# Kernel optimization log

Measured on AMD Instinct MI355X. Metric: run time of the kernel, lower is better.

Reference implementation:

```python
import jax, jax.numpy as jnp
import numpy as np
from jax import lax

HEADS, DIM_HEAD = 4, 64
INNER = HEADS * DIM_HEAD              # 256
FEAT_DIM = MAP_DIM = OUT_DIM = 128
EXPANDED = 4 * OUT_DIM                # 512 (MBConv expansion)
MAP_SIZE = (8, 8, 8)
EPS = 1e-5


def conv3d(x, w, groups=1):
    # x: NCDHW, w: OIDHW ([out, in/groups, kd, kh, kw]); stride 1, 'same' padding
    return lax.conv_general_dilated(x, w, (1, 1, 1), 'SAME',
                                    feature_group_count=groups,
                                    dimension_numbers=('NCDHW', 'OIDHW', 'NCDHW'))


def inorm(x):
    # InstanceNorm3d (affine=False): normalize over spatial dims per sample/channel
    m = x.mean((2, 3, 4), keepdims=True)
    v = ((x - m) ** 2).mean((2, 3, 4), keepdims=True)
    return (x - m) * lax.rsqrt(v + EPS)


def _split_heads(t, spatial):
    # 'b (dim_head heads) d h w -> b heads (d h w) dim_head'
    B = t.shape[0]
    N = spatial[0] * spatial[1] * spatial[2]
    return t.reshape(B, DIM_HEAD, HEADS, N).transpose(0, 2, 3, 1)


def _merge_heads(t, spatial):
    # 'b heads n dim_head -> b (dim_head heads) d h w'
    B = t.shape[0]
    return t.transpose(0, 3, 1, 2).reshape(B, DIM_HEAD * HEADS, *spatial)


def setup_inputs() -> dict:
    key = jax.random.key(0)
    ks = jax.random.split(key, 16)
    r = lambda k, s: jax.random.normal(k, s, jnp.float32) * 0.05
    return {
        'x': jax.random.normal(ks[0], (2, FEAT_DIM, 24, 24, 24), jnp.float32),
        'semantic_map': jax.random.normal(ks[1], (2, MAP_DIM) + MAP_SIZE, jnp.float32),
        'w_fqv_dw': r(ks[2], (FEAT_DIM, 1, 3, 3, 3)),
        'w_fqv_pw': r(ks[3], (2 * INNER, FEAT_DIM, 1, 1, 1)),
        'w_mqv':    r(ks[4], (2 * INNER, MAP_DIM, 1, 1, 1)),
        'w_fout_dw': r(ks[5], (INNER, 1, 3, 3, 3)),
        'w_fout_pw': r(ks[6], (OUT_DIM, INNER, 1, 1, 1)),
        'w_mout':   r(ks[7], (MAP_DIM, INNER, 1, 1, 1)),
        'w_exp':    r(ks[8], (EXPANDED, OUT_DIM, 1, 1, 1)),
        'w_dw':     r(ks[9], (EXPANDED, 1, 3, 3, 3)),
        'w_se1':    r(ks[10], (EXPANDED // 4, EXPANDED, 1, 1, 1)),
        'b_se1':    jnp.zeros((EXPANDED // 4,), jnp.float32),
        'w_se2':    r(ks[11], (EXPANDED, EXPANDED // 4, 1, 1, 1)),
        'b_se2':    jnp.zeros((EXPANDED,), jnp.float32),
        'w_pw':     r(ks[12], (OUT_DIM, EXPANDED, 1, 1, 1)),
    }


def _mbconv(x, w_exp, w_dw, w_se1, b_se1, w_se2, b_se2, w_pw):
    # MBConv (preact ConvNormAct blocks, InstanceNorm + ReLU, SE, identity shortcut)
    h = conv3d(jax.nn.relu(inorm(x)), w_exp)
    h = conv3d(jax.nn.relu(inorm(h)), w_dw, groups=EXPANDED)
    s = h.mean((2, 3, 4), keepdims=True)                       # squeeze
    s = jax.nn.relu(conv3d(s, w_se1) + b_se1[None, :, None, None, None])
    s = jax.nn.sigmoid(conv3d(s, w_se2) + b_se2[None, :, None, None, None])
    h = h * s
    h = conv3d(inorm(h), w_pw)                                 # pointwise, act=False
    return h + x


def reference(x, semantic_map, w_fqv_dw, w_fqv_pw, w_mqv, w_fout_dw, w_fout_pw,
              w_mout, w_exp, w_dw, w_se1, b_se1, w_se2, b_se2, w_pw):
    B, C, D, H, W = x.shape
    feat = inorm(x)
    m = inorm(semantic_map)

    # QV projections: depthwise-separable for feat, 1x1 for map
    fqv = conv3d(conv3d(feat, w_fqv_dw, groups=FEAT_DIM), w_fqv_pw)
    fq, fv = jnp.split(fqv, 2, axis=1)
    mqv = conv3d(m, w_mqv)
    mq, mv = jnp.split(mqv, 2, axis=1)

    fq = _split_heads(fq, (D, H, W))   # [B, h, Nf, dh]
    fv = _split_heads(fv, (D, H, W))
    mq = _split_heads(mq, MAP_SIZE)    # [B, h, Nm, dh]
    mv = _split_heads(mv, MAP_SIZE)

    # shared score matrix, dual-direction softmax
    attn = jnp.einsum('bhid,bhjd->bhij', fq, mq) * (DIM_HEAD ** -0.5)
    feat_map_attn = jax.nn.softmax(attn, axis=-1)   # over map tokens j
    map_feat_attn = jax.nn.softmax(attn, axis=-2)   # over feat tokens i

    feat_out = jnp.einsum('bhij,bhjd->bhid', feat_map_attn, mv)   # [B,h,Nf,dh]
    map_out = jnp.einsum('bhji,bhjd->bhid', map_feat_attn, fv)    # [B,h,Nm,dh]

    feat_out = _merge_heads(feat_out, (D, H, W))
    map_out = _merge_heads(map_out, MAP_SIZE)

    feat_out = conv3d(conv3d(feat_out, w_fout_dw, groups=INNER), w_fout_pw)
    map_out = conv3d(map_out, w_mout)

    out = feat_out + x   # shortcut is identity (feat_dim == out_dim)
    out = _mbconv(out, w_exp, w_dw, w_se1, b_se1, w_se2, b_se2, w_pw)
    map_out = map_out + semantic_map
    return out, map_out
```

## Files before the change

kernel.cpp:

```cpp
#include <hip/hip_runtime.h>
#include <hip/hip_bf16.h>
#include <cstddef>

#define NF 13824
#define NM 512
#define NIC 27

typedef __attribute__((ext_vector_type(8))) short bf16x8;
typedef __attribute__((ext_vector_type(4))) float f32x4;

__device__ __forceinline__ float fexp2(float x){ return __builtin_amdgcn_exp2f(x); }

__device__ __forceinline__ void gload16(const float* g, float* l){
  __builtin_amdgcn_global_load_lds((const __attribute__((address_space(1))) void*)g,
                                   (__attribute__((address_space(3))) void*)l, 16, 0, 0);
}

__global__ void k_transpose6(const float* __restrict__ s0, float* __restrict__ d0,
                             const float* __restrict__ s1, float* __restrict__ d1,
                             const float* __restrict__ s2, float* __restrict__ d2,
                             const float* __restrict__ s3, float* __restrict__ d3,
                             const float* __restrict__ s4, float* __restrict__ d4,
                             const float* __restrict__ s5, float* __restrict__ d5){
  const float* W; float* WT; int Cout, Cin;
  switch (blockIdx.y){
    case 0: W=s0; WT=d0; Cout=512; Cin=128; break;
    case 1: W=s1; WT=d1; Cout=512; Cin=128; break;
    case 2: W=s2; WT=d2; Cout=128; Cin=256; break;
    case 3: W=s3; WT=d3; Cout=128; Cin=256; break;
    case 4: W=s4; WT=d4; Cout=512; Cin=128; break;
    default: W=s5; WT=d5; Cout=128; Cin=512; break;
  }
  int idx = blockIdx.x*256 + threadIdx.x;
  if (idx >= Cout*Cin) return;
  int co = idx / Cin, ci = idx % Cin;
  WT[(size_t)ci*Cout + co] = W[idx];
}

__global__ void k_stats(const float* __restrict__ in, float2* __restrict__ st, int N,
                        float2* __restrict__ tf){
  int row = blockIdx.x;
  const float* p = in + (size_t)row*N;
  float s=0.f, q=0.f;
  int n4 = N/4;
  for (int i=threadIdx.x; i<n4; i+=256){
    float4 v = *(const float4*)(p + i*4);
    s += v.x+v.y+v.z+v.w;
    q += v.x*v.x+v.y*v.y+v.z*v.z+v.w*v.w;
  }
  __shared__ float rs[256], rq[256];
  rs[threadIdx.x]=s; rq[threadIdx.x]=q;
  __syncthreads();
  for (int o=128;o>0;o>>=1){
    if (threadIdx.x<o){ rs[threadIdx.x]+=rs[threadIdx.x+o]; rq[threadIdx.x]+=rq[threadIdx.x+o]; }
    __syncthreads();
  }
  if (threadIdx.x==0){
    float m = rs[0]/N;
    float v = rq[0]/N - m*m;
    if (v<0.f) v=0.f;
    st[row] = make_float2(m, v);
    if (tf){
      float a = rsqrtf(v + 1e-5f);
      tf[row] = make_float2(a, -m*a);
    }
  }
}

__global__ void k_make_tf(const float2* __restrict__ st, const float* __restrict__ sbuf,
                          float2* __restrict__ tf, int rows){
  int i = blockIdx.x*256 + threadIdx.x;
  if (i>=rows) return;
  float s = sbuf ? sbuf[i] : 1.f;
  float2 mv = st[i];
  float a = s*rsqrtf(s*s*mv.y + 1e-5f);
  tf[i] = make_float2(a, -mv.x*a);
}

__global__ void k_red(const float2* __restrict__ part, int nparts, int rows,
                      float invN, float2* __restrict__ tf){
  int w = threadIdx.x>>6, l = threadIdx.x&63;
  int row = blockIdx.x*4 + w;
  if (row >= rows) return;
  const float2* p = part + (size_t)row*nparts;
  float s=0.f, q=0.f;
  for (int k=l; k<nparts; k+=64){ float2 v = p[k]; s += v.x; q += v.y; }
  s += __shfl_xor(s,1); s += __shfl_xor(s,2); s += __shfl_xor(s,4);
  s += __shfl_xor(s,8); s += __shfl_xor(s,16); s += __shfl_xor(s,32);
  q += __shfl_xor(q,1); q += __shfl_xor(q,2); q += __shfl_xor(q,4);
  q += __shfl_xor(q,8); q += __shfl_xor(q,16); q += __shfl_xor(q,32);
  if (l==0){
    float m = s*invN;
    float v = q*invN - m*m;
    if (v<0.f) v=0.f;
    float a = rsqrtf(v + 1e-5f);
    tf[row] = make_float2(a, -m*a);
  }
}

__global__ void k_act(const float* __restrict__ in, const float2* __restrict__ tf,
                      float* __restrict__ outp){
  int i = blockIdx.x*256 + threadIdx.x;
  int n4 = i*4;
  int bc = n4 / NF;
  float2 t = tf[bc];
  float4 v = *(const float4*)(in + n4);
  v.x = fmaxf(t.x*v.x + t.y, 0.f);
  v.y = fmaxf(t.x*v.y + t.y, 0.f);
  v.z = fmaxf(t.x*v.z + t.y, 0.f);
  v.w = fmaxf(t.x*v.w + t.y, 0.f);
  *(float4*)(outp + n4) = v;
}

__global__ void k_fold(const float* __restrict__ wt, const float2* __restrict__ tf,
                       float* __restrict__ wf, float* __restrict__ bias){
  int co = blockIdx.x;
  int b  = blockIdx.y;
  float partb = 0.f;
  for (int ci=threadIdx.x; ci<512; ci+=256){
    float w = wt[ci*128 + co];
    float2 t = tf[b*512 + ci];
    wf[((size_t)b*512 + ci)*128 + co] = w * t.x;
    partb += w * t.y;
  }
  __shared__ float red[256];
  red[threadIdx.x] = partb; __syncthreads();
  for (int o=128;o>0;o>>=1){ if (threadIdx.x<o) red[threadIdx.x]+=red[threadIdx.x+o]; __syncthreads(); }
  if (threadIdx.x==0) bias[b*128 + co] = red[0];
}

__global__ __launch_bounds__(256) void k_dw3t(const float* __restrict__ in, const float* __restrict__ w,
                      const float2* __restrict__ tf, float* __restrict__ out,
                      int C, int relu, float2* __restrict__ stout){
  int bc = blockIdx.x;
  int c = bc % C;
  __shared__ float lds[4 + 26*728];
  __shared__ float rs2[256], rq2[256];
  float a = 1.f, bb = 0.f;
  if (tf){ float2 t = tf[bc]; a=t.x; bb=t.y; }

  {
    float4* l4 = (float4*)lds;
    float4 z = make_float4(0.f,0.f,0.f,0.f);
    for (int i=threadIdx.x; i<(4+26*728)/4; i+=256) l4[i] = z;
  }
  __syncthreads();

  const float* pin = in + (size_t)bc*NF;
  for (int i=threadIdx.x; i<NF/4; i+=256){
    int n = i*4;
    int d = n/576, r2 = n%576;
    int h = r2/24, wq = r2%24;
    float4 v = *(const float4*)(pin + n);
    float v0 = a*v.x+bb, v1 = a*v.y+bb, v2 = a*v.z+bb, v3 = a*v.w+bb;
    if (relu){ v0=fmaxf(v0,0.f); v1=fmaxf(v1,0.f); v2=fmaxf(v2,0.f); v3=fmaxf(v3,0.f); }
    *(float4*)(lds + 4 + (d+1)*728 + (h+1)*28 + wq) = make_float4(v0,v1,v2,v3);
  }

  const float* wc = w + c*27;
  float wr[27];
  #pragma unroll
  for (int k=0;k<27;k++) wr[k] = wc[k];
  __syncthreads();

  float ss=0.f, sq=0.f;
  for (int r = threadIdx.x; r < 576; r += 256){
    int d = r/24, h = r%24;
    float acc[24];
    #pragma unroll
    for (int i=0;i<24;i++) acc[i] = 0.f;
    #pragma unroll
    for (int kd=0;kd<3;kd++){
      #pragma unroll
      for (int kh=0;kh<3;kh++){
        const float* row = lds + 4 + (d+kd)*728 + (h+kh)*28;
        float rr[24];
        #pragma unroll
        for (int q=0;q<6;q++){
          float4 v4 = *(const float4*)(row + 4*q);
          rr[4*q]=v4.x; rr[4*q+1]=v4.y; rr[4*q+2]=v4.z; rr[4*q+3]=v4.w;
        }
        float rl = row[-1];
        float rrgt = row[24];
        float w0 = wr[kd*9+kh*3+0], w1 = wr[kd*9+kh*3+1], w2 = wr[kd*9+kh*3+2];
        acc[0] += w0*rl + w1*rr[0] + w2*rr[1];
        #pragma unroll
        for (int i=1;i<23;i++) acc[i] += w0*rr[i-1] + w1*rr[i] + w2*rr[i+1];
        acc[23] += w0*rr[22] + w1*rr[23] + w2*rrgt;
      }
    }
    if (stout){
      #pragma unroll
      for (int i=0;i<24;i++){ ss += acc[i]; sq += acc[i]*acc[i]; }
    }
    float* op = out + (size_t)bc*NF + r*24;
    #pragma unroll
    for (int q=0;q<6;q++)
      *(float4*)(op + 4*q) = make_float4(acc[4*q],acc[4*q+1],acc[4*q+2],acc[4*q+3]);
  }
  if (stout){
    rs2[threadIdx.x]=ss; rq2[threadIdx.x]=sq;
    __syncthreads();
    for (int o=128;o>0;o>>=1){
      if (threadIdx.x<o){ rs2[threadIdx.x]+=rs2[threadIdx.x+o]; rq2[threadIdx.x]+=rq2[threadIdx.x+o]; }
      __syncthreads();
    }
    if (threadIdx.x==0){
      float m = rs2[0]/NF;
      float v = rq2[0]/NF - m*m;
      stout[bc] = make_float2(m, v>0.f? v:0.f);
    }
  }
}

__global__ __launch_bounds__(256) void k_pw2(const float* __restrict__ in, const float* __restrict__ Wt,
                    const float* __restrict__ bias,
                    int Cin, int Cout, int N, int wstride,
                    const float* __restrict__ res,
                    float* __restrict__ out0,
                    __hip_bfloat16* __restrict__ qnm, __hip_bfloat16* __restrict__ vdm,
                    int mode, float2* __restrict__ part, int nparts){
  int b = blockIdx.z;
  int n0 = blockIdx.x*64, co0 = blockIdx.y*128;
  int t = threadIdx.x;
  int tx = t & 15, tyy = t >> 4;
  int wv = t >> 6, ln = t & 63;
  __shared__ float wl[2][32*128];
  __shared__ float il[2][32*64];
  float acc[8][4] = {};
  const float* inb = in + (size_t)b*Cin*N;
  const float* wb  = Wt + (size_t)b*wstride;

  int wrow = (ln>>5), wcol = (ln&31)*4;
  int irow = (ln>>4), icol = (ln&15)*4;

  auto STAGE = [&](int c0, int buf){
    #pragma unroll
    for (int k=0;k<4;k++){
      int row = wv*8 + 2*k + wrow;
      gload16(wb + (size_t)(c0+row)*Cout + co0 + wcol, &wl[buf][row*128 + wcol]);
    }
    #pragma unroll
    for (int k=0;k<2;k++){
      int row = wv*8 + 4*k + irow;
      gload16(inb + (size_t)(c0+row)*N + n0 + icol, &il[buf][row*64 + icol]);
    }
  };

  STAGE(0, 0);
  __syncthreads();

  int nc = Cin >> 5;
  int cur = 0;
  for (int c=0; c<nc; c++){
    if (c+1 < nc) STAGE((c+1)*32, cur^1);
    #pragma unroll
    for (int ci=0;ci<32;ci++){
      const float* wr2 = &wl[cur][ci*128 + tyy*8];
      float4 w0 = *(const float4*)(wr2);
      float4 w1 = *(const float4*)(wr2+4);
      float4 b4 = *(const float4*)&il[cur][ci*64 + tx*4];
      acc[0][0]+=w0.x*b4.x; acc[0][1]+=w0.x*b4.y; acc[0][2]+=w0.x*b4.z; acc[0][3]+=w0.x*b4.w;
      acc[1][0]+=w0.y*b4.x; acc[1][1]+=w0.y*b4.y; acc[1][2]+=w0.y*b4.z; acc[1][3]+=w0.y*b4.w;
      acc[2][0]+=w0.z*b4.x; acc[2][1]+=w0.z*b4.y; acc[2][2]+=w0.z*b4.z; acc[2][3]+=w0.z*b4.w;
      acc[3][0]+=w0.w*b4.x; acc[3][1]+=w0.w*b4.y; acc[3][2]+=w0.w*b4.z; acc[3][3]+=w0.w*b4.w;
      acc[4][0]+=w1.x*b4.x; acc[4][1]+=w1.x*b4.y; acc[4][2]+=w1.x*b4.z; acc[4][3]+=w1.x*b4.w;
      acc[5][0]+=w1.y*b4.x; acc[5][1]+=w1.y*b4.y; acc[5][2]+=w1.y*b4.z; acc[5][3]+=w1.y*b4.w;
      acc[6][0]+=w1.z*b4.x; acc[6][1]+=w1.z*b4.y; acc[6][2]+=w1.z*b4.z; acc[6][3]+=w1.z*b4.w;
      acc[7][0]+=w1.w*b4.x; acc[7][1]+=w1.w*b4.y; acc[7][2]+=w1.w*b4.z; acc[7][3]+=w1.w*b4.w;
    }
    __syncthreads();
    cur ^= 1;
  }

  if (mode==0){
    #pragma unroll
    for (int i=0;i<8;i++){
      int co = co0 + tyy*8 + i;
      float bco = bias ? bias[b*Cout + co] : 0.f;
      float* op = out0 + ((size_t)b*Cout + co)*N;
      float sv=0.f, qv=0.f;
      #pragma unroll
      for (int j=0;j<4;j++){
        int n = n0 + tx*4 + j;
        float v = acc[i][j] + bco;
        if (res) v += res[((size_t)b*Cout + co)*N + n];
        op[n] = v;
        sv += v; qv += v*v;
      }
      if (part){
        sv += __shfl_xor(sv,1); sv += __shfl_xor(sv,2); sv += __shfl_xor(sv,4); sv += __shfl_xor(sv,8);
        qv += __shfl_xor(qv,1); qv += __shfl_xor(qv,2); qv += __shfl_xor(qv,4); qv += __shfl_xor(qv,8);
        if (tx==0)
          part[(size_t)(b*Cout + co)*nparts + blockIdx.x] = make_float2(sv, qv);
      }
    }
  } else {
    bool isq = (co0 < 256);
    #pragma unroll
    for (int i=0;i<8;i++){
      int co = co0 + tyy*8 + i;
      int head = co & 3, dd = (co & 255) >> 2;
      int bhid = b*4 + head;
      #pragma unroll
      for (int j=0;j<4;j++){
        int n = n0 + tx*4 + j;
        __hip_bfloat16 v = __float2bfloat16(acc[i][j]);
        if (isq) qnm[((size_t)bhid*N + n)*64 + dd] = v;
        else     vdm[((size_t)(bhid*64 + dd))*N + n] = v;
      }
    }
  }
}

__global__ __launch_bounds__(256) void k_pw2s(const float* __restrict__ in, const float* __restrict__ Wt,
                    const float* __restrict__ bias,
                    int Cin, int Cout, int N, int wstride,
                    const float* __restrict__ res,
                    float* __restrict__ out0,
                    int mode, float2* __restrict__ part, int nparts){
  int b = blockIdx.z;
  int n0 = blockIdx.x*64, co0 = blockIdx.y*64;
  int t = threadIdx.x;
  int tx = t & 15, ty = t >> 4;
  int wv = t >> 6, ln = t & 63;
  __shared__ float wl[2][32*64];
  __shared__ float il[2][32*64];
  float acc[4][4] = {};
  const float* inb = in + (size_t)b*Cin*N;
  const float* wb  = Wt + (size_t)b*wstride;

  int row4 = (ln>>4), col4 = (ln&15)*4;

  auto STAGE = [&](int c0, int buf){
    #pragma unroll
    for (int k=0;k<2;k++){
      int row = wv*8 + 4*k + row4;
      gload16(wb  + (size_t)(c0+row)*Cout + co0 + col4, &wl[buf][row*64 + col4]);
      gload16(inb + (size_t)(c0+row)*N    + n0  + col4, &il[buf][row*64 + col4]);
    }
  };

  STAGE(0, 0);
  __syncthreads();

  int nc = Cin >> 5;
  int cur = 0;
  for (int c=0; c<nc; c++){
    if (c+1 < nc) STAGE((c+1)*32, cur^1);
    #pragma unroll
    for (int ci=0;ci<32;ci++){
      float4 a4 = *(const float4*)&wl[cur][ci*64 + ty*4];
      float4 b4 = *(const float4*)&il[cur][ci*64 + tx*4];
      acc[0][0]+=a4.x*b4.x; acc[0][1]+=a4.x*b4.y; acc[0][2]+=a4.x*b4.z; acc[0][3]+=a4.x*b4.w;
      acc[1][0]+=a4.y*b4.x; acc[1][1]+=a4.y*b4.y; acc[1][2]+=a4.y*b4.z; acc[1][3]+=a4.y*b4.w;
      acc[2][0]+=a4.z*b4.x; acc[2][1]+=a4.z*b4.y; acc[2][2]+=a4.z*b4.z; acc[2][3]+=a4.z*b4.w;
      acc[3][0]+=a4.w*b4.x; acc[3][1]+=a4.w*b4.y; acc[3][2]+=a4.w*b4.z; acc[3][3]+=a4.w*b4.w;
    }
    __syncthreads();
    cur ^= 1;
  }

  #pragma unroll
  for (int i=0;i<4;i++){
    int co = co0 + ty*4 + i;
    float bco = bias ? bias[b*Cout + co] : 0.f;
    float* op = out0 + ((size_t)b*Cout + co)*N;
    float sv=0.f, qv=0.f;
    #pragma unroll
    for (int j=0;j<4;j++){
      int n = n0 + tx*4 + j;
      float v = acc[i][j] + bco;
      if (res) v += res[((size_t)b*Cout + co)*N + n];
      op[n] = v;
      sv += v; qv += v*v;
    }
    if (part){
      sv += __shfl_xor(sv,1); sv += __shfl_xor(sv,2); sv += __shfl_xor(sv,4); sv += __shfl_xor(sv,8);
      qv += __shfl_xor(qv,1); qv += __shfl_xor(qv,2); qv += __shfl_xor(qv,4); qv += __shfl_xor(qv,8);
      if (tx==0)
        part[(size_t)(b*Cout + co)*nparts + blockIdx.x] = make_float2(sv, qv);
    }
  }
  (void)mode;
}

__global__ __launch_bounds__(256) void k_pw(const float* __restrict__ in, const float* __restrict__ WT,
                    const float2* __restrict__ tf, int relu,
                    int Cin, int Cout, int N,
                    const float* __restrict__ res,
                    float* __restrict__ out0,
                    __hip_bfloat16* __restrict__ qnm, __hip_bfloat16* __restrict__ vdm,
                    int mode){
  int b = blockIdx.z;
  int n0 = blockIdx.x*64, co0 = blockIdx.y*64;
  int tx = threadIdx.x & 15, ty = threadIdx.x >> 4;
  int cc = threadIdx.x & 63, g = threadIdx.x >> 6;
  __shared__ float wl[32][68];
  __shared__ float il[32][68];
  float acc[4][4] = {};
  const float* inb = in + (size_t)b*Cin*N;

  float rw[8], rv[8], ta[8], tb[8];
  #pragma unroll
  for (int rr=0;rr<8;rr++){ ta[rr]=1.f; tb[rr]=0.f; }
  #pragma unroll
  for (int rr=0;rr<8;rr++){
    int ci = g + 4*rr;
    rw[rr] = WT[(size_t)ci*Cout + co0 + cc];
    rv[rr] = inb[(size_t)ci*N + n0 + cc];
    if (tf){ float2 t = tf[b*Cin + ci]; ta[rr]=t.x; tb[rr]=t.y; }
  }

  for (int c0=0;c0<Cin;c0+=32){
    __syncthreads();
    #pragma unroll
    for (int rr=0;rr<8;rr++){
      int ci = g + 4*rr;
      wl[ci][cc] = rw[rr];
      float v = ta[rr]*rv[rr] + tb[rr];
      if (relu) v = fmaxf(v, 0.f);
      il[ci][cc] = v;
    }
    __syncthreads();
    if (c0+32 < Cin){
      int c0n = c0+32;
      #pragma unroll
      for (int rr=0;rr<8;rr++){
        int ci = g + 4*rr;
        rw[rr] = WT[(size_t)(c0n+ci)*Cout + co0 + cc];
        rv[rr] = inb[(size_t)(c0n+ci)*N + n0 + cc];
        if (tf){ float2 t = tf[b*Cin + c0n + ci]; ta[rr]=t.x; tb[rr]=t.y; }
      }
    }
    #pragma unroll
    for (int ci=0;ci<32;ci++){
      float4 a4 = *(const float4*)&wl[ci][ty*4];
      float4 b4 = *(const float4*)&il[ci][tx*4];
      acc[0][0]+=a4.x*b4.x; acc[0][1]+=a4.x*b4.y; acc[0][2]+=a4.x*b4.z; acc[0][3]+=a4.x*b4.w;
      acc[1][0]+=a4.y*b4.x; acc[1][1]+=a4.y*b4.y; acc[1][2]+=a4.y*b4.z; acc[1][3]+=a4.y*b4.w;
      acc[2][0]+=a4.z*b4.x; acc[2][1]+=a4.z*b4.y; acc[2][2]+=a4.z*b4.z; acc[2][3]+=a4.z*b4.w;
      acc[3][0]+=a4.w*b4.x; acc[3][1]+=a4.w*b4.y; acc[3][2]+=a4.w*b4.z; acc[3][3]+=a4.w*b4.w;
    }
  }
  if (mode==0){
    #pragma unroll
    for (int i=0;i<4;i++){
      int co = co0 + ty*4 + i;
      float* op = out0 + ((size_t)b*Cout + co)*N;
      #pragma unroll
      for (int j=0;j<4;j++){
        int n = n0 + tx*4 + j;
        float v = acc[i][j];
        if (res) v += res[((size_t)b*Cout + co)*N + n];
        op[n] = v;
      }
    }
  } else {
    int ccbase = (co0 & 255) + ty*4;
    int dd = ccbase >> 2;
    bool isq = (co0 < 256);
    #pragma unroll
    for (int i=0;i<4;i++){
      int bhid = b*4 + i;
      #pragma unroll
      for (int j=0;j<4;j++){
        int n = n0 + tx*4 + j;
        __hip_bfloat16 v = __float2bfloat16(acc[i][j]);
        if (isq) qnm[((size_t)bhid*N + n)*64 + dd] = v;
        else     vdm[((size_t)(bhid*64 + dd))*N + n] = v;
      }
    }
  }
}

__global__ __launch_bounds__(256) void k_attn(const __hip_bfloat16* __restrict__ qf,
    const __hip_bfloat16* __restrict__ qm, const __hip_bfloat16* __restrict__ vm,
    const __hip_bfloat16* __restrict__ vf,
    float* __restrict__ fo, float* __restrict__ num, float* __restrict__ cs){
  __shared__ __hip_bfloat16 pl[4][2][16][40];
  __shared__ float rsl[4][32];
  int bid = blockIdx.x;
  int sub = bid >> 1;
  int w = threadIdx.x>>6, l = threadIdx.x&63;
  int lr = l&15, lg = l>>4;

  if (bid & 1){
    int bh = sub/108, b = bh>>2, h = bh&3;
    int i0 = (sub%108)*128 + w*32;
    bf16x8 aq[2][2];
    #pragma unroll
    for (int g=0; g<2; g++){
      const __hip_bfloat16* qb = qf + ((size_t)bh*NF + i0 + g*16 + lr)*64 + lg*8;
      aq[g][0] = *(const bf16x8*)(qb);
      aq[g][1] = *(const bf16x8*)(qb + 32);
    }
    f32x4 facc[2][4];
    #pragma unroll
    for (int g=0; g<2; g++)
      #pragma unroll
      for (int t=0;t<4;t++){ facc[g][t][0]=0.f; facc[g][t][1]=0.f; facc[g][t][2]=0.f; facc[g][t][3]=0.f; }
    float rs[2][4] = {};
    const __hip_bfloat16* kbase = qm + ((size_t)bh*NM + lr)*64 + lg*8;
    const __hip_bfloat16* vbase = vm + ((size_t)bh*64 + lr)*NM + lg*8;

    auto fcomp = [&](bf16x8 K0, bf16x8 K1, bf16x8 K2, bf16x8 K3,
                     bf16x8 V0, bf16x8 V1, bf16x8 V2, bf16x8 V3){
      #pragma unroll
      for (int g=0; g<2; g++){
        f32x4 s0 = {0.f,0.f,0.f,0.f}, s1 = {0.f,0.f,0.f,0.f};
        s0 = __builtin_amdgcn_mfma_f32_16x16x32_bf16(aq[g][0], K0, s0, 0,0,0);
        s0 = __builtin_amdgcn_mfma_f32_16x16x32_bf16(aq[g][1], K1, s0, 0,0,0);
        s1 = __builtin_amdgcn_mfma_f32_16x16x32_bf16(aq[g][0], K2, s1, 0,0,0);
        s1 = __builtin_amdgcn_mfma_f32_16x16x32_bf16(aq[g][1], K3, s1, 0,0,0);
        #pragma unroll
        for (int r=0;r<4;r++){
          float p0 = fexp2(s0[r]*0.18033688f);
          float p1 = fexp2(s1[r]*0.18033688f);
          pl[w][g][4*lg+r][lr]    = __float2bfloat16(p0);
          pl[w][g][4*lg+r][16+lr] = __float2bfloat16(p1);
          rs[g][r] += p0 + p1;
        }
      }
      #pragma unroll
      for (int g=0; g<2; g++){
        bf16x8 bp = *(const bf16x8*)&pl[w][g][lr][lg*8];
        facc[g][0] = __builtin_amdgcn_mfma_f32_16x16x32_bf16(V0, bp, facc[g][0], 0,0,0);
        facc[g][1] = __builtin_amdgcn_mfma_f32_16x16x32_bf16(V1, bp, facc[g][1], 0,0,0);
        facc[g][2] = __builtin_amdgcn_mfma_f32_16x16x32_bf16(V2, bp, facc[g][2], 0,0,0);
        facc[g][3] = __builtin_amdgcn_mfma_f32_16x16x32_bf16(V3, bp, facc[g][3], 0,0,0);
      }
    };

    bf16x8 kA0,kA1,kA2,kA3,vA0,vA1,vA2,vA3;
    bf16x8 kB0,kB1,kB2,kB3,vB0,vB1,vB2,vB3;
    #define FLOAD(KP,VP,J0) \
      KP##0 = *(const bf16x8*)(kbase + (size_t)(J0)*64); \
      KP##1 = *(const bf16x8*)(kbase + (size_t)(J0)*64 + 32); \
      KP##2 = *(const bf16x8*)(kbase + (size_t)(J0)*64 + 1024); \
      KP##3 = *(const bf16x8*)(kbase + (size_t)(J0)*64 + 1056); \
      VP##0 = *(const bf16x8*)(vbase + (J0)); \
      VP##1 = *(const bf16x8*)(vbase + 16*NM + (J0)); \
      VP##2 = *(const bf16x8*)(vbase + 32*NM + (J0)); \
      VP##3 = *(const bf16x8*)(vbase + 48*NM + (J0));

    FLOAD(kA,vA,0)
    for (int jt=0; jt<16; jt+=2){
      FLOAD(kB,vB,(jt+1)*32)
      fcomp(kA0,kA1,kA2,kA3,vA0,vA1,vA2,vA3);
      if (jt+2 < 16){ FLOAD(kA,vA,(jt+2)*32) }
      fcomp(kB0,kB1,kB2,kB3,vB0,vB1,vB2,vB3);
    }
    #undef FLOAD

    #pragma unroll
    for (int g=0; g<2; g++)
      #pragma unroll
      for (int r=0;r<4;r++){
        float v = rs[g][r];
        v += __shfl_xor(v,1); v += __shfl_xor(v,2); v += __shfl_xor(v,4); v += __shfl_xor(v,8);
        if (lr==0) rsl[w][g*16 + 4*lg+r] = v;
      }
    __syncthreads();
    #pragma unroll
    for (int g=0; g<2; g++){
      float inv = 1.f / rsl[w][g*16 + lr];
      #pragma unroll
      for (int dt=0; dt<4; dt++){
        #pragma unroll
        for (int r=0;r<4;r++){
          int d = dt*16 + 4*lg + r;
          fo[((size_t)(b*256 + d*4 + h))*NF + i0 + g*16 + lr] = facc[g][dt][r]*inv;
        }
      }
    }
  } else {
    int ic = sub%27, jb = (sub/27)&3, bh = sub/108;
    int jt0 = jb*128 + w*16;
    int jt1 = jt0 + 64;
    bf16x8 am[2][2];
    {
      const __hip_bfloat16* ab0 = qm + ((size_t)bh*NM + jt0 + lr)*64 + lg*8;
      const __hip_bfloat16* ab1 = qm + ((size_t)bh*NM + jt1 + lr)*64 + lg*8;
      am[0][0] = *(const bf16x8*)(ab0);
      am[0][1] = *(const bf16x8*)(ab0 + 32);
      am[1][0] = *(const bf16x8*)(ab1);
      am[1][1] = *(const bf16x8*)(ab1 + 32);
    }
    f32x4 macc[2][4];
    #pragma unroll
    for (int jg=0;jg<2;jg++)
      #pragma unroll
      for (int t=0;t<4;t++){ macc[jg][t][0]=0.f; macc[jg][t][1]=0.f; macc[jg][t][2]=0.f; macc[jg][t][3]=0.f; }
    float csr[2][4] = {};
    const __hip_bfloat16* fbase  = qf + ((size_t)bh*NF + lr)*64 + lg*8;
    const __hip_bfloat16* vfbase = vf + ((size_t)bh*64 + lr)*NF + lg*8;

    auto mcomp = [&](bf16x8 F0, bf16x8 F1, bf16x8 F2, bf16x8 F3,
                     bf16x8 V0, bf16x8 V1, bf16x8 V2, bf16x8 V3){
      #pragma unroll
      for (int jg=0;jg<2;jg++){
        f32x4 s0 = {0.f,0.f,0.f,0.f}, s1 = {0.f,0.f,0.f,0.f};
        s0 = __builtin_amdgcn_mfma_f32_16x16x32_bf16(am[jg][0], F0, s0, 0,0,0);
        s0 = __builtin_amdgcn_mfma_f32_16x16x32_bf16(am[jg][1], F1, s0, 0,0,0);
        s1 = __builtin_amdgcn_mfma_f32_16x16x32_bf16(am[jg][0], F2, s1, 0,0,0);
        s1 = __builtin_amdgcn_mfma_f32_16x16x32_bf16(am[jg][1], F3, s1, 0,0,0);
        #pragma unroll
        for (int r=0;r<4;r++){
          float p0 = fexp2(s0[r]*0.18033688f);
          float p1 = fexp2(s1[r]*0.18033688f);
          pl[w][jg][4*lg+r][lr]    = __float2bfloat16(p0);
          pl[w][jg][4*lg+r][16+lr] = __float2bfloat16(p1);
          csr[jg][r] += p0 + p1;
        }
      }
      #pragma unroll
      for (int jg=0;jg<2;jg++){
        bf16x8 bp = *(const bf16x8*)&pl[w][jg][lr][lg*8];
        macc[jg][0] = __builtin_amdgcn_mfma_f32_16x16x32_bf16(V0, bp, macc[jg][0], 0,0,0);
        macc[jg][1] = __builtin_amdgcn_mfma_f32_16x16x32_bf16(V1, bp, macc[jg][1], 0,0,0);
        macc[jg][2] = __builtin_amdgcn_mfma_f32_16x16x32_bf16(V2, bp, macc[jg][2], 0,0,0);
        macc[jg][3] = __builtin_amdgcn_mfma_f32_16x16x32_bf16(V3, bp, macc[jg][3], 0,0,0);
      }
    };

    bf16x8 fA0,fA1,fA2,fA3,vA0,vA1,vA2,vA3;
    bf16x8 fB0,fB1,fB2,fB3,vB0,vB1,vB2,vB3;
    #define MLOAD(FP,VP,I0) \
      FP##0 = *(const bf16x8*)(fbase + (size_t)(I0)*64); \
      FP##1 = *(const bf16x8*)(fbase + (size_t)(I0)*64 + 32); \
      FP##2 = *(const bf16x8*)(fbase + (size_t)(I0)*64 + 1024); \
      FP##3 = *(const bf16x8*)(fbase + (size_t)(I0)*64 + 1056); \
      VP##0 = *(const bf16x8*)(vfbase + (size_t)(I0)); \
      VP##1 = *(const bf16x8*)(vfbase + (size_t)16*NF + (I0)); \
      VP##2 = *(const bf16x8*)(vfbase + (size_t)32*NF + (I0)); \
      VP##3 = *(const bf16x8*)(vfbase + (size_t)48*NF + (I0));

    int ibase = ic*512;
    MLOAD(fA,vA, ibase)
    for (int is=0; is<16; is+=2){
      MLOAD(fB,vB, ibase + (is+1)*32)
      mcomp(fA0,fA1,fA2,fA3,vA0,vA1,vA2,vA3);
      if (is+2<16){ MLOAD(fA,vA, ibase + (is+2)*32) }
      mcomp(fB0,fB1,fB2,fB3,vB0,vB1,vB2,vB3);
    }
    #undef MLOAD

    size_t nb = ((size_t)(ic*8 + bh)*64)*512;
    #pragma unroll
    for (int jg=0;jg<2;jg++){
      int jt = jg ? jt1 : jt0;
      #pragma unroll
      for (int dt=0;dt<4;dt++){
        #pragma unroll
        for (int r=0;r<4;r++){
          num[nb + (size_t)(dt*16 + 4*lg + r)*512 + jt + lr] = macc[jg][dt][r];
        }
      }
    }
    #pragma unroll
    for (int jg=0;jg<2;jg++){
      int jt = jg ? jt1 : jt0;
      #pragma unroll
      for (int r=0;r<4;r++){
        float v = csr[jg][r];
        v += __shfl_xor(v,1); v += __shfl_xor(v,2); v += __shfl_xor(v,4); v += __shfl_xor(v,8);
        if (lr==0) cs[(size_t)(ic*8 + bh)*512 + jt + 4*lg + r] = v;
      }
    }
  }
}

__global__ void k_comb(const float* __restrict__ num, const float* __restrict__ cs,
                       float* __restrict__ ma){
  int idx = blockIdx.x*256 + threadIdx.x;
  if (idx >= 8*512*64) return;
  int bh = idx>>15; int rem = idx&32767; int d = rem>>9; int j = rem&511;
  float s=0.f, c=0.f;
  for (int ic=0;ic<NIC;ic++){
    s += num[((size_t)(ic*8+bh)*64 + d)*512 + j];
    c += cs[(size_t)(ic*8+bh)*512 + j];
  }
  int b = bh>>2, h = bh&3;
  ma[((size_t)(b*256 + d*4 + h))*NM + j] = s/c;
}

__global__ void k_se(const float2* __restrict__ st, const float* __restrict__ w1, const float* __restrict__ b1,
                     const float* __restrict__ w2, const float* __restrict__ b2, float* __restrict__ sout){
  int b = blockIdx.x; int t = threadIdx.x;
  __shared__ float mean[512]; __shared__ float s1[128];
  mean[t]     = st[b*512 + t].x;
  mean[t+256] = st[b*512 + t + 256].x;
  __syncthreads();
  if (t<128){
    float a = b1[t];
    for (int c=0;c<512;c++) a += w1[t*512+c]*mean[c];
    s1[t] = fmaxf(a, 0.f);
  }
  __syncthreads();
  for (int o=t;o<512;o+=256){
    float a = b2[o];
    for (int c=0;c<128;c++) a += w2[o*128+c]*s1[c];
    sout[b*512+o] = 1.f/(1.f+__expf(-a));
  }
}

extern "C" void kernel_launch(void* const* d_in, const int* in_sizes, int n_in,
                              void* d_out, int out_size, void* d_ws, size_t ws_size,
                              hipStream_t stream){
  const float* x     = (const float*)d_in[0];
  const float* smap  = (const float*)d_in[1];
  const float* wfdw  = (const float*)d_in[2];
  const float* wfpw  = (const float*)d_in[3];
  const float* wmqv  = (const float*)d_in[4];
  const float* wodw  = (const float*)d_in[5];
  const float* wopw  = (const float*)d_in[6];
  const float* wmout = (const float*)d_in[7];
  const float* wexp  = (const float*)d_in[8];
  const float* wdw   = (const float*)d_in[9];
  const float* wse1  = (const float*)d_in[10];
  const float* bse1  = (const float*)d_in[11];
  const float* wse2  = (const float*)d_in[12];
  const float* bse2  = (const float*)d_in[13];
  const float* wpw   = (const float*)d_in[14];

  float* out  = (float*)d_out;
  float* mout = out + (size_t)2*128*NF;

  float* W = (float*)d_ws;
  size_t o = 0;
  __hip_bfloat16* qf = (__hip_bfloat16*)(W + o); o += (size_t)8*NF*32;
  __hip_bfloat16* vf = (__hip_bfloat16*)(W + o); o += (size_t)8*NF*32;
  float* fdw  = W + o; o += (size_t)2*128*NF;
  float* num  = W + o; o += (size_t)NIC*8*64*512;
  __hip_bfloat16* qm = (__hip_bfloat16*)(W + o); o += 8*NM*32;
  __hip_bfloat16* vm = (__hip_bfloat16*)(W + o); o += 8*NM*32;
  float* csb  = W + o; o += (size_t)NIC*8*512;
  float* ma   = W + o; o += (size_t)2*256*NM;
  float* h2   = (float*)d_ws;
  float* fo   = W + o; o += (size_t)2*256*NF;
  float* fdw2 = W + o; o += (size_t)2*256*NF;
  float* h1 = fo;
  float* wTf  = W + o; o += 512*128;
  float* wTm  = W + o; o += 512*128;
  float* wTo  = W + o; o += 128*256;
  float* wTmo = W + o; o += 128*256;
  float* wTe  = W + o; o += 512*128;
  float* wTp  = W + o; o += 128*512;
  float* wfP  = W + o; o += (size_t)2*512*128;
  float* biasP= W + o; o += 2*128;
  float2* partO = (float2*)(W+o); o += (size_t)2*256*216;
  float2* partH1= (float2*)(W+o); o += (size_t)2*1024*216;
  float2* tfO = (float2*)(W+o); o += 512;
  float2* tfH1= (float2*)(W+o); o += 2048;
  float2* stA = (float2*)(W+o); o += 512;
  float2* tfA = (float2*)(W+o); o += 512;
  float2* stM = (float2*)(W+o); o += 512;
  float2* tfM = (float2*)(W+o); o += 512;
  float2* stH2= (float2*)(W+o); o += 2048;
  float2* tfH = (float2*)(W+o); o += 2048;
  float* sbuf = W + o; o += 1024;
  (void)ws_size; (void)in_sizes; (void)n_in; (void)out_size;

  k_transpose6<<<dim3(256,6),256,0,stream>>>(wfpw,wTf, wmqv,wTm, wopw,wTo, wmout,wTmo, wexp,wTe, wpw,wTp);

  k_stats<<<256,256,0,stream>>>(x, stA, NF, tfA);
  k_dw3t<<<256,256,0,stream>>>(x, wfdw, tfA, fdw, 128, 0, nullptr);
  k_pw2<<<dim3(216,4,2),256,0,stream>>>(fdw, wTf, nullptr, 128,512,NF,0, nullptr, nullptr, qf, vf, 1, nullptr,0);

  k_stats<<<256,256,0,stream>>>(smap, stM, NM, tfM);
  k_pw<<<dim3(8,8,2),256,0,stream>>>(smap, wTm, tfM,0, 128,512,NM, nullptr, nullptr, qm, vm, 1);

  k_attn<<<dim3(1728),256,0,stream>>>(qf, qm, vm, vf, fo, num, csb);
  k_comb<<<1024,256,0,stream>>>(num, csb, ma);

  k_dw3t<<<512,256,0,stream>>>(fo, wodw, nullptr, fdw2, 256, 0, nullptr);
  k_pw2s<<<dim3(216,2,2),256,0,stream>>>(fdw2, wTo, nullptr, 256,128,NF,0, x, out, 0, partO,216);
  k_pw<<<dim3(8,2,2),256,0,stream>>>(ma, wTmo, nullptr,0, 256,128,NM, smap, mout, nullptr,nullptr, 0);

  k_red<<<64,256,0,stream>>>(partO, 216, 256, 1.f/NF, tfO);
  k_act<<<3456,256,0,stream>>>(out, tfO, fdw);
  k_pw2<<<dim3(216,4,2),256,0,stream>>>(fdw, wTe, nullptr, 128,512,NF,0, nullptr, h1, nullptr,nullptr, 0, partH1,216);

  k_red<<<256,256,0,stream>>>(partH1, 216, 1024, 1.f/NF, tfH1);
  k_dw3t<<<1024,256,0,stream>>>(h1, wdw, tfH1, h2, 512, 1, stH2);

  k_se<<<2,256,0,stream>>>(stH2, wse1,bse1,wse2,bse2, sbuf);
  k_make_tf<<<4,256,0,stream>>>(stH2, sbuf, tfH, 1024);
  k_fold<<<dim3(128,2),256,0,stream>>>(wTp, tfH, wfP, biasP);
  k_pw2s<<<dim3(216,2,2),256,0,stream>>>(h2, wfP, biasP, 512,128,NF,512*128, out, out, 0, nullptr,0);
}
```

Before: 519.3 us.

## Split depthwise conv per channel into two depth halves; add MFMA setprio in attention

The depthwise 3x3x3 conv kernel now processes half of the depth slices per block (two blocks per channel). Each block loads 13 slices plus a zero halo into a smaller LDS tile, which raises block count and cuts LDS use per block so more blocks can be resident. Channel statistics are now written as per-half partial sums and combined by a new small finalize kernel. The attention compute lambdas also split MFMA score computation from the exp/softmax stage and wrap the MFMA sections in s_setprio to favour matrix issue. In exchange the conv reloads two halo slices per channel and adds one extra launch.

```diff
diff --git a/kernel.cpp b/kernel.cpp
--- a/kernel.cpp
+++ b/kernel.cpp
@@ -98,6 +98,17 @@
   }
 }
 
+__global__ void k_fin2(const float2* __restrict__ p, float2* __restrict__ st,
+                       int rows, float invN){
+  int i = blockIdx.x*256 + threadIdx.x;
+  if (i>=rows) return;
+  float2 a = p[2*i], b = p[2*i+1];
+  float s = a.x+b.x, q = a.y+b.y;
+  float m = s*invN;
+  float v = q*invN - m*m;
+  st[i] = make_float2(m, v>0.f? v:0.f);
+}
+
 __global__ void k_act(const float* __restrict__ in, const float2* __restrict__ tf,
                       float* __restrict__ outp){
   int i = blockIdx.x*256 + threadIdx.x;
@@ -129,12 +140,13 @@
   if (threadIdx.x==0) bias[b*128 + co] = red[0];
 }
 
-__global__ __launch_bounds__(256) void k_dw3t(const float* __restrict__ in, const float* __restrict__ w,
+__global__ __launch_bounds__(256) void k_dw3s(const float* __restrict__ in, const float* __restrict__ w,
                       const float2* __restrict__ tf, float* __restrict__ out,
-                      int C, int relu, float2* __restrict__ stout){
-  int bc = blockIdx.x;
+                      int C, int relu, float2* __restrict__ pstout){
+  int bid = blockIdx.x;
+  int half = bid & 1, bc = bid >> 1;
   int c = bc % C;
-  __shared__ float lds[4 + 26*728];
+  __shared__ float lds[4 + 14*728];
   __shared__ float rs2[256], rq2[256];
   float a = 1.f, bb = 0.f;
   if (tf){ float2 t = tf[bc]; a=t.x; bb=t.y; }
@@ -142,19 +154,22 @@
   {
     float4* l4 = (float4*)lds;
     float4 z = make_float4(0.f,0.f,0.f,0.f);
-    for (int i=threadIdx.x; i<(4+26*728)/4; i+=256) l4[i] = z;
+    for (int i=threadIdx.x; i<(4+14*728)/4; i+=256) l4[i] = z;
   }
   __syncthreads();
 
+  int base = half*12 - 1;
+  int dlo = half ? 11 : 0;
   const float* pin = in + (size_t)bc*NF;
-  for (int i=threadIdx.x; i<NF/4; i+=256){
+  for (int i=threadIdx.x; i<13*576/4; i+=256){
     int n = i*4;
-    int d = n/576, r2 = n%576;
+    int dl = n/576, r2 = n%576;
+    int d = dlo + dl;
     int h = r2/24, wq = r2%24;
-    float4 v = *(const float4*)(pin + n);
+    float4 v = *(const float4*)(pin + (size_t)d*576 + r2);
     float v0 = a*v.x+bb, v1 = a*v.y+bb, v2 = a*v.z+bb, v3 = a*v.w+bb;
     if (relu){ v0=fmaxf(v0,0.f); v1=fmaxf(v1,0.f); v2=fmaxf(v2,0.f); v3=fmaxf(v3,0.f); }
-    *(float4*)(lds + 4 + (d+1)*728 + (h+1)*28 + wq) = make_float4(v0,v1,v2,v3);
+    *(float4*)(lds + 4 + (d-base)*728 + (h+1)*28 + wq) = make_float4(v0,v1,v2,v3);
   }
 
   const float* wc = w + c*27;
@@ -164,8 +179,8 @@
   __syncthreads();
 
   float ss=0.f, sq=0.f;
-  for (int r = threadIdx.x; r < 576; r += 256){
-    int d = r/24, h = r%24;
+  for (int r = threadIdx.x; r < 288; r += 256){
+    int dl = r/24, h = r%24;
     float acc[24];
     #pragma unroll
     for (int i=0;i<24;i++) acc[i] = 0.f;
@@ -173,7 +188,7 @@
     for (int kd=0;kd<3;kd++){
       #pragma unroll
       for (int kh=0;kh<3;kh++){
-        const float* row = lds + 4 + (d+kd)*728 + (h+kh)*28;
+        const float* row = lds + 4 + (dl+kd)*728 + (h+kh)*28;
         float rr[24];
         #pragma unroll
         for (int q=0;q<6;q++){
@@ -189,27 +204,23 @@
         acc[23] += w0*rr[22] + w1*rr[23] + w2*rrgt;
       }
     }
-    if (stout){
+    if (pstout){
       #pragma unroll
       for (int i=0;i<24;i++){ ss += acc[i]; sq += acc[i]*acc[i]; }
     }
-    float* op = out + (size_t)bc*NF + r*24;
+    float* op = out + (size_t)bc*NF + (half*12 + dl)*576 + h*24;
     #pragma unroll
     for (int q=0;q<6;q++)
       *(float4*)(op + 4*q) = make_float4(acc[4*q],acc[4*q+1],acc[4*q+2],acc[4*q+3]);
   }
-  if (stout){
+  if (pstout){
     rs2[threadIdx.x]=ss; rq2[threadIdx.x]=sq;
     __syncthreads();
     for (int o=128;o>0;o>>=1){
       if (threadIdx.x<o){ rs2[threadIdx.x]+=rs2[threadIdx.x+o]; rq2[threadIdx.x]+=rq2[threadIdx.x+o]; }
       __syncthreads();
     }
-    if (threadIdx.x==0){
-      float m = rs2[0]/NF;
-      float v = rq2[0]/NF - m*m;
-      stout[bc] = make_float2(m, v>0.f? v:0.f);
-    }
+    if (threadIdx.x==0) pstout[bc*2 + half] = make_float2(rs2[0], rq2[0]);
   }
 }
 
@@ -506,6 +517,8 @@
 
     auto fcomp = [&](bf16x8 K0, bf16x8 K1, bf16x8 K2, bf16x8 K3,
                      bf16x8 V0, bf16x8 V1, bf16x8 V2, bf16x8 V3){
+      __builtin_amdgcn_s_setprio(1);
+      f32x4 s[2][2];
       #pragma unroll
       for (int g=0; g<2; g++){
         f32x4 s0 = {0.f,0.f,0.f,0.f}, s1 = {0.f,0.f,0.f,0.f};
@@ -513,15 +526,21 @@
         s0 = __builtin_amdgcn_mfma_f32_16x16x32_bf16(aq[g][1], K1, s0, 0,0,0);
         s1 = __builtin_amdgcn_mfma_f32_16x16x32_bf16(aq[g][0], K2, s1, 0,0,0);
         s1 = __builtin_amdgcn_mfma_f32_16x16x32_bf16(aq[g][1], K3, s1, 0,0,0);
+        s[g][0] = s0; s[g][1] = s1;
+      }
+      __builtin_amdgcn_s_setprio(0);
+      #pragma unroll
+      for (int g=0; g<2; g++){
         #pragma unroll
         for (int r=0;r<4;r++){
-          float p0 = fexp2(s0[r]*0.18033688f);
-          float p1 = fexp2(s1[r]*0.18033688f);
+          float p0 = fexp2(s[g][0][r]*0.18033688f);
+          float p1 = fexp2(s[g][1][r]*0.18033688f);
           pl[w][g][4*lg+r][lr]    = __float2bfloat16(p0);
           pl[w][g][4*lg+r][16+lr] = __float2bfloat16(p1);
           rs[g][r] += p0 + p1;
         }
       }
+      __builtin_amdgcn_s_setprio(1);
       #pragma unroll
       for (int g=0; g<2; g++){
         bf16x8 bp = *(const bf16x8*)&pl[w][g][lr][lg*8];
@@ -530,6 +549,7 @@
         facc[g][2] = __builtin_amdgcn_mfma_f32_16x16x32_bf16(V2, bp, facc[g][2], 0,0,0);
         facc[g][3] = __builtin_amdgcn_mfma_f32_16x16x32_bf16(V3, bp, facc[g][3], 0,0,0);
       }
+      __builtin_amdgcn_s_setprio(0);
     };
 
     bf16x8 kA0,kA1,kA2,kA3,vA0,vA1,vA2,vA3;
@@ -598,6 +618,8 @@
 
     auto mcomp = [&](bf16x8 F0, bf16x8 F1, bf16x8 F2, bf16x8 F3,
                      bf16x8 V0, bf16x8 V1, bf16x8 V2, bf16x8 V3){
+      __builtin_amdgcn_s_setprio(1);
+      f32x4 s[2][2];
       #pragma unroll
       for (int jg=0;jg<2;jg++){
         f32x4 s0 = {0.f,0.f,0.f,0.f}, s1 = {0.f,0.f,0.f,0.f};
@@ -605,15 +627,21 @@
         s0 = __builtin_amdgcn_mfma_f32_16x16x32_bf16(am[jg][1], F1, s0, 0,0,0);
         s1 = __builtin_amdgcn_mfma_f32_16x16x32_bf16(am[jg][0], F2, s1, 0,0,0);
         s1 = __builtin_amdgcn_mfma_f32_16x16x32_bf16(am[jg][1], F3, s1, 0,0,0);
+        s[jg][0] = s0; s[jg][1] = s1;
+      }
+      __builtin_amdgcn_s_setprio(0);
+      #pragma unroll
+      for (int jg=0;jg<2;jg++){
         #pragma unroll
         for (int r=0;r<4;r++){
-          float p0 = fexp2(s0[r]*0.18033688f);
-          float p1 = fexp2(s1[r]*0.18033688f);
+          float p0 = fexp2(s[jg][0][r]*0.18033688f);
+          float p1 = fexp2(s[jg][1][r]*0.18033688f);
           pl[w][jg][4*lg+r][lr]    = __float2bfloat16(p0);
           pl[w][jg][4*lg+r][16+lr] = __float2bfloat16(p1);
           csr[jg][r] += p0 + p1;
         }
       }
+      __builtin_amdgcn_s_setprio(1);
       #pragma unroll
       for (int jg=0;jg<2;jg++){
         bf16x8 bp = *(const bf16x8*)&pl[w][jg][lr][lg*8];
@@ -622,6 +650,7 @@
         macc[jg][2] = __builtin_amdgcn_mfma_f32_16x16x32_bf16(V2, bp, macc[jg][2], 0,0,0);
         macc[jg][3] = __builtin_amdgcn_mfma_f32_16x16x32_bf16(V3, bp, macc[jg][3], 0,0,0);
       }
+      __builtin_amdgcn_s_setprio(0);
     };
 
     bf16x8 fA0,fA1,fA2,fA3,vA0,vA1,vA2,vA3;
@@ -751,6 +780,7 @@
   float* biasP= W + o; o += 2*128;
   float2* partO = (float2*)(W+o); o += (size_t)2*256*216;
   float2* partH1= (float2*)(W+o); o += (size_t)2*1024*216;
+  float2* pstH2 = (float2*)(W+o); o += 4096;
   float2* tfO = (float2*)(W+o); o += 512;
   float2* tfH1= (float2*)(W+o); o += 2048;
   float2* stA = (float2*)(W+o); o += 512;
@@ -765,7 +795,7 @@
   k_transpose6<<<dim3(256,6),256,0,stream>>>(wfpw,wTf, wmqv,wTm, wopw,wTo, wmout,wTmo, wexp,wTe, wpw,wTp);
 
   k_stats<<<256,256,0,stream>>>(x, stA, NF, tfA);
-  k_dw3t<<<256,256,0,stream>>>(x, wfdw, tfA, fdw, 128, 0, nullptr);
+  k_dw3s<<<512,256,0,stream>>>(x, wfdw, tfA, fdw, 128, 0, nullptr);
   k_pw2<<<dim3(216,4,2),256,0,stream>>>(fdw, wTf, nullptr, 128,512,NF,0, nullptr, nullptr, qf, vf, 1, nullptr,0);
 
   k_stats<<<256,256,0,stream>>>(smap, stM, NM, tfM);
@@ -774,7 +804,7 @@
   k_attn<<<dim3(1728),256,0,stream>>>(qf, qm, vm, vf, fo, num, csb);
   k_comb<<<1024,256,0,stream>>>(num, csb, ma);
 
-  k_dw3t<<<512,256,0,stream>>>(fo, wodw, nullptr, fdw2, 256, 0, nullptr);
+  k_dw3s<<<1024,256,0,stream>>>(fo, wodw, nullptr, fdw2, 256, 0, nullptr);
   k_pw2s<<<dim3(216,2,2),256,0,stream>>>(fdw2, wTo, nullptr, 256,128,NF,0, x, out, 0, partO,216);
   k_pw<<<dim3(8,2,2),256,0,stream>>>(ma, wTmo, nullptr,0, 256,128,NM, smap, mout, nullptr,nullptr, 0);
 
@@ -783,7 +813,8 @@
   k_pw2<<<dim3(216,4,2),256,0,stream>>>(fdw, wTe, nullptr, 128,512,NF,0, nullptr, h1, nullptr,nullptr, 0, partH1,216);
 
   k_red<<<256,256,0,stream>>>(partH1, 216, 1024, 1.f/NF, tfH1);
-  k_dw3t<<<1024,256,0,stream>>>(h1, wdw, tfH1, h2, 512, 1, stH2);
+  k_dw3s<<<2048,256,0,stream>>>(h1, wdw, tfH1, h2, 512, 1, pstH2);
+  k_fin2<<<4,256,0,stream>>>(pstH2, stH2, 1024, 1.f/NF);
 
   k_se<<<2,256,0,stream>>>(stH2, wse1,bse1,wse2,bse2, sbuf);
   k_make_tf<<<4,256,0,stream>>>(stH2, sbuf, tfH, 1024);
```

Result: no change. 527.8 us (+1.6%).
